# Performance work log

Hardware: AMD Instinct MI355X
Metric: run time of the kernel (lower is better)

Reference implementation:

```python
import jax, jax.numpy as jnp
import numpy as np

B, L, DIM = 4, 2048, 512
H, D = 8, 64
SCALE = D ** -0.5
NEG = -10000.0


def setup_inputs() -> dict:
    key = jax.random.key(0)
    ks = jax.random.split(key, 5)
    std = 1.0 / np.sqrt(DIM)
    return {
        "x": jax.random.normal(ks[0], (B, L, DIM), dtype=jnp.float32),
        "wq": jax.random.normal(ks[1], (H * D, DIM), dtype=jnp.float32) * std,
        "wk": jax.random.normal(ks[2], (H * D, DIM), dtype=jnp.float32) * std,
        "wv": jax.random.normal(ks[3], (H * D, DIM), dtype=jnp.float32) * std,
        "wo": jax.random.normal(ks[4], (DIM, H * D), dtype=jnp.float32) * std,
    }


def reference(x, wq, wk, wv, wo):
    b, l, _ = x.shape
    # projections (torch Linear: y = x @ W.T), split heads -> [b,h,l,d]
    q = (x @ wq.T).reshape(b, l, H, D).transpose(0, 2, 1, 3)
    k = (x @ wk.T).reshape(b, l, H, D).transpose(0, 2, 1, 3)
    v = (x @ wv.T).reshape(b, l, H, D).transpose(0, 2, 1, 3)
    scores = jnp.einsum("bhld,bhsd->bhls", q, k) * SCALE
    scores = jnp.nan_to_num(scores, nan=0.0, posinf=10000.0, neginf=NEG)
    diag = jnp.eye(l, dtype=bool)[None, None]  # [1,1,l,l]
    scores = jnp.where(diag, NEG, scores)
    attn = jax.nn.softmax(scores, axis=-1)
    attn = jnp.where(diag, 0.0, attn)
    attn = jnp.nan_to_num(attn, nan=0.0, posinf=0.0, neginf=0.0)
    out = jnp.einsum("bhls,bhsd->bhld", attn, v)
    out = out.transpose(0, 2, 1, 3).reshape(b, l, H * D)
    return out @ wo.T
```

## Files before the change

kernel.cpp:

```cpp
#include <hip/hip_runtime.h>
#include <hip/hip_bf16.h>


#define Bsz 4
#define Lsz 2048
#define DIMsz 512
#define Hsz 8
#define Dsz 64

typedef _Float16 f16;
typedef __attribute__((ext_vector_type(8))) _Float16 f16x8;
typedef __attribute__((ext_vector_type(4))) _Float16 f16x4;
typedef __attribute__((ext_vector_type(2))) __fp16 fp16x2;
typedef __attribute__((ext_vector_type(4))) float f32x4;
typedef __attribute__((ext_vector_type(16))) float f32x16;
typedef unsigned int u32;
typedef __attribute__((ext_vector_type(2))) unsigned int u32x2;

#if __has_builtin(__builtin_amdgcn_exp2f)
#define EXP2(x) __builtin_amdgcn_exp2f(x)
#else
#define EXP2(x) __expf(0.6931471805599453f * (x))
#endif

__device__ __forceinline__ u32 pack2(float a, float b) {
#if __has_builtin(__builtin_amdgcn_cvt_pkrtz)
    fp16x2 h = __builtin_amdgcn_cvt_pkrtz(a, b);
    return __builtin_bit_cast(u32, h);
#else
    fp16x2 h; h.x = (__fp16)a; h.y = (__fp16)b;
    return __builtin_bit_cast(u32, h);
#endif
}

#if __has_builtin(__builtin_amdgcn_permlane32_swap)
__device__ __forceinline__ void plswap(u32& a, u32& b) {
    u32x2 r = __builtin_amdgcn_permlane32_swap(a, b, false, false);
    a = r.x; b = r.y;
}
#else
__device__ __forceinline__ void plswap(u32& a, u32& b) {
    u32 sa = (u32)__shfl_xor((int)a, 32);
    u32 sb = (u32)__shfl_xor((int)b, 32);
    bool hi = (threadIdx.x & 32) != 0;
    u32 na = hi ? sb : a;
    u32 nb = hi ? b : sa;
    a = na; b = nb;
}
#endif

__device__ __forceinline__ void gl2lds16(const void* g, void* l) {
    __builtin_amdgcn_global_load_lds(
        (const __attribute__((address_space(1))) u32*)g,
        (__attribute__((address_space(3))) u32*)l, 16, 0, 0);
}

__global__ __launch_bounds__(256) void pack_f16(
    const float* __restrict__ x, const float* __restrict__ wq,
    const float* __restrict__ wk, const float* __restrict__ wv,
    const float* __restrict__ wo,
    f16* __restrict__ xh, f16* __restrict__ w3h, f16* __restrict__ woh)
{
    int bx = blockIdx.x, seg, blk;
    if (bx < 4096) { seg = 0; blk = bx; }
    else { seg = 1 + ((bx - 4096) >> 8); blk = (bx - 4096) & 255; }
    const float* s; f16* d; float sc = 1.0f;
    switch (seg) {
        case 0: s = x;  d = xh;            break;
        case 1: s = wq; d = w3h;           sc = 0.18033688011112042f; break;
        case 2: s = wk; d = w3h + 262144;  break;
        case 3: s = wv; d = w3h + 524288;  break;
        default: s = wo; d = woh;          break;
    }
    int i = (blk * 256 + threadIdx.x) * 4;
    float4 v = *(const float4*)(s + i);
    f16x4 o;
    o.x = (f16)(v.x * sc); o.y = (f16)(v.y * sc);
    o.z = (f16)(v.z * sc); o.w = (f16)(v.w * sc);
    *(f16x4*)(d + i) = o;
}

__global__ __launch_bounds__(256) void gemm_qkv_f16(
    const f16* __restrict__ A, const f16* __restrict__ B,
    f16* __restrict__ qh, f16* __restrict__ kh, f16* __restrict__ vth)
{
    __shared__ __align__(16) char smem[32768];
    f16* Ash = (f16*)smem;
    f16* Bsh = (f16*)(smem + 16384);

    const int tid = threadIdx.x;
    const int w = tid >> 6, lane = tid & 63;
    const int quad = lane >> 4, low = lane & 15;
    const int wm = w >> 1, wn = w & 1;
    const int m0 = blockIdx.y * 128, n0 = blockIdx.x * 128;

    f32x4 acc[4][4];
    #pragma unroll
    for (int i = 0; i < 4; i++)
        #pragma unroll
        for (int j = 0; j < 4; j++) acc[i][j] = (f32x4){0.f, 0.f, 0.f, 0.f};

    #pragma unroll 1
    for (int k0 = 0; k0 < DIMsz; k0 += 64) {
        __syncthreads();
        #pragma unroll
        for (int j = 0; j < 4; j++) {
            int t = j * 256 + tid;
            int r = t >> 3, g = t & 7;
            int gc = (g ^ (r & 7)) * 8;
            char* lb = (char*)Ash + (j * 256 + w * 64) * 16;
            gl2lds16(A + (size_t)(m0 + r) * DIMsz + k0 + gc, lb);
            char* lb2 = (char*)Bsh + (j * 256 + w * 64) * 16;
            gl2lds16(B + (size_t)(n0 + r) * DIMsz + k0 + gc, lb2);
        }
        __syncthreads();

        #pragma unroll
        for (int ks2 = 0; ks2 < 2; ks2++) {
            f16x8 af[4], bf[4];
            #pragma unroll
            for (int mt = 0; mt < 4; mt++) {
                int ar = wm * 64 + mt * 16 + low;
                int c = ks2 * 4 + quad;
                af[mt] = *(const f16x8*)&Ash[ar * 64 + ((c ^ (ar & 7)) << 3)];
            }
            #pragma unroll
            for (int nt = 0; nt < 4; nt++) {
                int br = wn * 64 + nt * 16 + low;
                int c = ks2 * 4 + quad;
                bf[nt] = *(const f16x8*)&Bsh[br * 64 + ((c ^ (br & 7)) << 3)];
            }
            #pragma unroll
            for (int mt = 0; mt < 4; mt++)
                #pragma unroll
                for (int nt = 0; nt < 4; nt++)
                    acc[mt][nt] = __builtin_amdgcn_mfma_f32_16x16x32_f16(
                        af[mt], bf[nt], acc[mt][nt], 0, 0, 0);
        }
    }

    const int proj = n0 >> 9;
    if (proj < 2) {
        f16* dst = (proj == 0) ? qh : kh;
        #pragma unroll
        for (int nt = 0; nt < 4; nt++) {
            int n = n0 + wn * 64 + nt * 16 + low;
            int c = n & 511, h = c >> 6, d = c & 63;
            #pragma unroll
            for (int mt = 0; mt < 4; mt++)
                #pragma unroll
                for (int r = 0; r < 4; r++) {
                    int m = m0 + wm * 64 + mt * 16 + quad * 4 + r;
                    int b_ = m >> 11, l = m & (Lsz - 1);
                    size_t bh = (size_t)(b_ * Hsz + h);
                    dst[(bh * Lsz + l) * Dsz + d] = (f16)acc[mt][nt][r];
                }
        }
    } else {
        const int hb = (n0 & 511) >> 6;
        f16* Tv = (f16*)smem;
        const int b_ = m0 >> 11, l0 = m0 & (Lsz - 1);
        #pragma unroll 1
        for (int hs = 0; hs < 2; hs++) {
            __syncthreads();
            if (wn == hs) {
                #pragma unroll
                for (int nt = 0; nt < 4; nt++) {
                    int d = nt * 16 + low;
                    #pragma unroll
                    for (int mt = 0; mt < 4; mt++)
                        #pragma unroll
                        for (int r = 0; r < 4; r++) {
                            int l = wm * 64 + mt * 16 + quad * 4 + r;
                            Tv[d * 136 + l] = (f16)acc[mt][nt][r];
                        }
                }
            }
            __syncthreads();
            int d = tid >> 2, seg = tid & 3;
            size_t bh = (size_t)(b_ * Hsz + hb + hs);
            f16* dstp = vth + (bh * 64 + d) * (size_t)Lsz + l0 + seg * 32;
            const f16* srcp = Tv + d * 136 + seg * 32;
            #pragma unroll
            for (int j = 0; j < 4; j++)
                *(f16x8*)(dstp + j * 8) = *(const f16x8*)(srcp + j * 8);
        }
    }
}

__global__ __launch_bounds__(256, 3) void attn_mfma(
    const f16* __restrict__ q, const f16* __restrict__ k,
    const f16* __restrict__ vt, f16* __restrict__ ctx)
{
    __shared__ __align__(16) char smem[32768];
    __shared__ float Ls[4][2][32];

    f16* Ks = (f16*)smem;
    f16* Vs = (f16*)(smem + 16384);

    const int tid = threadIdx.x;
    const int w = tid >> 6, lane = tid & 63;
    const int col = lane & 31;
    const int h = lane >> 5;
    const int bh = blockIdx.x;
    const int qb = blockIdx.y;
    const int q0 = qb * 64;
    const size_t kvb = (size_t)bh * Lsz;

    f16x8 qf[2][4];
    #pragma unroll
    for (int qt = 0; qt < 2; qt++)
        #pragma unroll
        for (int s = 0; s < 4; s++)
            qf[qt][s] = *(const f16x8*)(q + (kvb + q0 + qt * 32 + col) * Dsz
                                          + s * 16 + h * 8);

    const f16* kp; const f16* vp;
    {
        int rk = tid >> 3, gk = tid & 7;
        kp = k + (kvb + rk) * Dsz + ((gk ^ (rk & 7)) << 3);
        int rv = tid >> 4, gv = tid & 15;
        vp = vt + ((size_t)bh * Dsz + rv) * Lsz + ((gv ^ (rv & 15)) << 3);
    }
    char* kl = (char*)Ks + (w * 64) * 16;
    char* vl = (char*)Vs + (w * 64) * 16;

    const int rk = w * 32 + col;
    const f16* kfp[4];
    #pragma unroll
    for (int s = 0; s < 4; s++)
        kfp[s] = Ks + rk * 64 + (((s * 2 + h) ^ (rk & 7)) << 3);
    const f16* vfp[2][2];
    #pragma unroll
    for (int dt = 0; dt < 2; dt++)
        #pragma unroll
        for (int ks = 0; ks < 2; ks++) {
            int rv = dt * 32 + col, cv = w * 4 + ks * 2 + h;
            vfp[dt][ks] = Vs + rv * 128 + ((cv ^ (rv & 15)) << 3);
        }

    f32x16 acc[2][2];
    #pragma unroll
    for (int qt = 0; qt < 2; qt++)
        #pragma unroll
        for (int dt = 0; dt < 2; dt++)
            #pragma unroll
            for (int i = 0; i < 16; i++) acc[qt][dt][i] = 0.f;
    float lsum[2] = {0.f, 0.f};

    const int drd_s0 = (qb >> 1) * 128;
    const int dqt = w - (qb & 1) * 2;

    #pragma unroll 1
    for (int s0 = 0; s0 < Lsz; s0 += 128) {
        __syncthreads();
        gl2lds16(kp,        kl);
        gl2lds16(kp + 2048, kl + 4096);
        gl2lds16(kp + 4096, kl + 8192);
        gl2lds16(kp + 6144, kl + 12288);
        gl2lds16(vp,            vl);
        gl2lds16(vp + 16 * Lsz, vl + 4096);
        gl2lds16(vp + 32 * Lsz, vl + 8192);
        gl2lds16(vp + 48 * Lsz, vl + 12288);
        kp += 128 * Dsz;
        vp += 128;
        __syncthreads();

        f32x16 st[2];
        #pragma unroll
        for (int i = 0; i < 16; i++) { st[0][i] = 0.f; st[1][i] = 0.f; }
        #pragma unroll
        for (int s = 0; s < 4; s++) {
            f16x8 kf = *(const f16x8*)kfp[s];
            st[0] = __builtin_amdgcn_mfma_f32_32x32x16_f16(kf, qf[0][s], st[0], 0, 0, 0);
            st[1] = __builtin_amdgcn_mfma_f32_32x32x16_f16(kf, qf[1][s], st[1], 0, 0, 0);
        }

        union { u32 u[4]; f16x8 v; } pf[2][2];
        const bool drnd = (s0 == drd_s0);
        #pragma unroll
        for (int qt = 0; qt < 2; qt++) {
            float pv[16];
            #pragma unroll
            for (int i = 0; i < 16; i++) pv[i] = EXP2(st[qt][i]);
            if (drnd && qt == dqt) {
                #pragma unroll
                for (int i = 0; i < 16; i++) {
                    int row = (i & 3) + 8 * (i >> 2) + 4 * h;
                    pv[i] = (row == col) ? 0.f : pv[i];
                }
            }
            #pragma unroll
            for (int i = 0; i < 16; i++) lsum[qt] += pv[i];
            u32 P2[8];
            #pragma unroll
            for (int j = 0; j < 8; j++)
                P2[j] = pack2(pv[2 * j], pv[2 * j + 1]);
            plswap(P2[0], P2[2]); plswap(P2[1], P2[3]);
            plswap(P2[4], P2[6]); plswap(P2[5], P2[7]);
            #pragma unroll
            for (int jj = 0; jj < 4; jj++) {
                pf[qt][0].u[jj] = P2[jj];
                pf[qt][1].u[jj] = P2[4 + jj];
            }
        }

        #pragma unroll
        for (int dt = 0; dt < 2; dt++)
            #pragma unroll
            for (int ks = 0; ks < 2; ks++) {
                f16x8 vf = *(const f16x8*)vfp[dt][ks];
                acc[0][dt] = __builtin_amdgcn_mfma_f32_32x32x16_f16(
                    vf, pf[0][ks].v, acc[0][dt], 0, 0, 0);
                acc[1][dt] = __builtin_amdgcn_mfma_f32_32x32x16_f16(
                    vf, pf[1][ks].v, acc[1][dt], 0, 0, 0);
            }
    }

    #pragma unroll
    for (int qt = 0; qt < 2; qt++) {
        lsum[qt] += __shfl_xor(lsum[qt], 32);
        if (h == 0) Ls[w][qt][col] = lsum[qt];
    }

    float* Om = (float*)smem;
    __syncthreads();
    if (w == 1 || w == 3) {
        float* og = Om + (w >> 1) * 4096;
        #pragma unroll
        for (int qt = 0; qt < 2; qt++)
            #pragma unroll
            for (int dt = 0; dt < 2; dt++)
                #pragma unroll
                for (int i = 0; i < 16; i++) {
                    int row = (i & 3) + 8 * (i >> 2) + 4 * h;
                    og[(dt * 32 + row) * 64 + qt * 32 + col] = acc[qt][dt][i];
                }
    }
    __syncthreads();
    if (w == 0 || w == 2) {
        const float* og = Om + (w >> 1) * 4096;
        #pragma unroll
        for (int qt = 0; qt < 2; qt++)
            #pragma unroll
            for (int dt = 0; dt < 2; dt++)
                #pragma unroll
                for (int i = 0; i < 16; i++) {
                    int row = (i & 3) + 8 * (i >> 2) + 4 * h;
                    acc[qt][dt][i] += og[(dt * 32 + row) * 64 + qt * 32 + col];
                }
    }
    __syncthreads();
    if (w == 2) {
        #pragma unroll
        for (int qt = 0; qt < 2; qt++)
            #pragma unroll
            for (int dt = 0; dt < 2; dt++)
                #pragma unroll
                for (int i = 0; i < 16; i++) {
                    int row = (i & 3) + 8 * (i >> 2) + 4 * h;
                    Om[(dt * 32 + row) * 64 + qt * 32 + col] = acc[qt][dt][i];
                }
    }
    __syncthreads();
    if (w == 0) {
        #pragma unroll
        for (int qt = 0; qt < 2; qt++)
            #pragma unroll
            for (int dt = 0; dt < 2; dt++)
                #pragma unroll
                for (int i = 0; i < 16; i++) {
                    int row = (i & 3) + 8 * (i >> 2) + 4 * h;
                    acc[qt][dt][i] += Om[(dt * 32 + row) * 64 + qt * 32 + col];
                }
        const int b = bh >> 3, hh = bh & 7;
        #pragma unroll
        for (int qt = 0; qt < 2; qt++) {
            float ls = Ls[0][qt][col] + Ls[1][qt][col]
                     + Ls[2][qt][col] + Ls[3][qt][col];
            const float inv = 1.0f / ls;
            f16* op = ctx + ((size_t)(b * Lsz + q0 + qt * 32 + col)) * DIMsz
                          + hh * 64;
            #pragma unroll
            for (int dt = 0; dt < 2; dt++)
                #pragma unroll
                for (int r4 = 0; r4 < 4; r4++) {
                    f16x4 o;
                    o.x = (f16)(acc[qt][dt][4 * r4 + 0] * inv);
                    o.y = (f16)(acc[qt][dt][4 * r4 + 1] * inv);
                    o.z = (f16)(acc[qt][dt][4 * r4 + 2] * inv);
                    o.w = (f16)(acc[qt][dt][4 * r4 + 3] * inv);
                    *(f16x4*)(op + dt * 32 + 8 * r4 + 4 * h) = o;
                }
        }
    }
}

__global__ __launch_bounds__(256) void gemm_out_f16(
    const f16* __restrict__ A, const f16* __restrict__ B,
    float* __restrict__ C)
{
    __shared__ f16 Ash[64 * 64];
    __shared__ f16 Bsh[64 * 64];
    const int tid = threadIdx.x;
    const int w = tid >> 6, lane = tid & 63;
    const int quad = lane >> 4, low = lane & 15;
    const int wm = w >> 1, wn = w & 1;
    const int m0 = blockIdx.y * 64, n0 = blockIdx.x * 64;

    f32x4 acc[2][2];
    #pragma unroll
    for (int i = 0; i < 2; i++)
        #pragma unroll
        for (int j = 0; j < 2; j++) acc[i][j] = (f32x4){0.f, 0.f, 0.f, 0.f};

    #pragma unroll 1
    for (int k0 = 0; k0 < DIMsz; k0 += 64) {
        __syncthreads();
        #pragma unroll
        for (int j = 0; j < 2; j++) {
            int t = j * 256 + tid;
            int r = t >> 3, g = t & 7;
            int gc = (g ^ (r & 7)) * 8;
            char* lb = (char*)Ash + (j * 256 + w * 64) * 16;
            gl2lds16(A + (size_t)(m0 + r) * DIMsz + k0 + gc, lb);
            char* lb2 = (char*)Bsh + (j * 256 + w * 64) * 16;
            gl2lds16(B + (size_t)(n0 + r) * DIMsz + k0 + gc, lb2);
        }
        __syncthreads();

        #pragma unroll
        for (int ks2 = 0; ks2 < 2; ks2++) {
            f16x8 af[2], bf[2];
            #pragma unroll
            for (int mt = 0; mt < 2; mt++) {
                int ar = wm * 32 + mt * 16 + low;
                int c = ks2 * 4 + quad;
                af[mt] = *(const f16x8*)&Ash[ar * 64 + ((c ^ (ar & 7)) << 3)];
            }
            #pragma unroll
            for (int nt = 0; nt < 2; nt++) {
                int br = wn * 32 + nt * 16 + low;
                int c = ks2 * 4 + quad;
                bf[nt] = *(const f16x8*)&Bsh[br * 64 + ((c ^ (br & 7)) << 3)];
            }
            #pragma unroll
            for (int mt = 0; mt < 2; mt++)
                #pragma unroll
                for (int nt = 0; nt < 2; nt++)
                    acc[mt][nt] = __builtin_amdgcn_mfma_f32_16x16x32_f16(
                        af[mt], bf[nt], acc[mt][nt], 0, 0, 0);
        }
    }

    #pragma unroll
    for (int mt = 0; mt < 2; mt++)
        #pragma unroll
        for (int r = 0; r < 4; r++) {
            int m = m0 + wm * 32 + mt * 16 + quad * 4 + r;
            #pragma unroll
            for (int nt = 0; nt < 2; nt++) {
                int n = n0 + wn * 32 + nt * 16 + low;
                C[(size_t)m * DIMsz + n] = acc[mt][nt][r];
            }
        }
}

extern "C" void kernel_launch(void* const* d_in, const int* in_sizes, int n_in,
                              void* d_out, int out_size, void* d_ws, size_t ws_size,
                              hipStream_t stream) {
    const float* x  = (const float*)d_in[0];
    const float* wq = (const float*)d_in[1];
    const float* wk = (const float*)d_in[2];
    const float* wv = (const float*)d_in[3];
    const float* wo = (const float*)d_in[4];
    float* out = (float*)d_out;

    const size_t NTOK = (size_t)Bsz * Lsz;
    const size_t XSZ  = NTOK * DIMsz;

    f16* xh   = (f16*)d_ws;
    f16* w3h  = xh + XSZ;
    f16* woh  = w3h + 3 * 262144;
    f16* qh   = woh + 262144;
    f16* kh   = qh + XSZ;
    f16* vth  = kh + XSZ;
    f16* ctxh = vth + XSZ;

    pack_f16<<<5120, 256, 0, stream>>>(x, wq, wk, wv, wo, xh, w3h, woh);

    dim3 g1(1536 / 128, NTOK / 128);
    gemm_qkv_f16<<<g1, 256, 0, stream>>>(xh, w3h, qh, kh, vth);

    dim3 g2(Bsz * Hsz, Lsz / 64);
    attn_mfma<<<g2, 256, 0, stream>>>(qh, kh, vth, ctxh);

    dim3 g3(DIMsz / 64, NTOK / 64);
    gemm_out_f16<<<g3, 256, 0, stream>>>(ctxh, woh, out);
}
```

Baseline: 166.6 us.

## Double-buffer K/V LDS tiles in attention and sum probabilities via fdot2

```diff
diff --git a/kernel.cpp b/kernel.cpp
--- a/kernel.cpp
+++ b/kernel.cpp
@@ -30,6 +30,16 @@
 #else
     fp16x2 h; h.x = (__fp16)a; h.y = (__fp16)b;
     return __builtin_bit_cast(u32, h);
+#endif
+}
+
+__device__ __forceinline__ float addpair(u32 p, float c) {
+#if __has_builtin(__builtin_amdgcn_fdot2)
+    fp16x2 ones; ones.x = (__fp16)1.0f; ones.y = (__fp16)1.0f;
+    return __builtin_amdgcn_fdot2(__builtin_bit_cast(fp16x2, p), ones, c, false);
+#else
+    fp16x2 h = __builtin_bit_cast(fp16x2, p);
+    return c + (float)h.x + (float)h.y;
 #endif
 }
 
@@ -188,15 +198,12 @@
     }
 }
 
-__global__ __launch_bounds__(256, 3) void attn_mfma(
+__global__ __launch_bounds__(256, 2) void attn_mfma(
     const f16* __restrict__ q, const f16* __restrict__ k,
     const f16* __restrict__ vt, f16* __restrict__ ctx)
 {
-    __shared__ __align__(16) char smem[32768];
+    __shared__ __align__(16) char smem[65536];
     __shared__ float Ls[4][2][32];
-
-    f16* Ks = (f16*)smem;
-    f16* Vs = (f16*)(smem + 16384);
 
     const int tid = threadIdx.x;
     const int w = tid >> 6, lane = tid & 63;
@@ -222,22 +229,28 @@
         int rv = tid >> 4, gv = tid & 15;
         vp = vt + ((size_t)bh * Dsz + rv) * Lsz + ((gv ^ (rv & 15)) << 3);
     }
-    char* kl = (char*)Ks + (w * 64) * 16;
-    char* vl = (char*)Vs + (w * 64) * 16;
-
+
+    char* kl[2]; char* vl[2];
+    const f16* kfp[2][4];
+    const f16* vfp[2][2][2];
     const int rk = w * 32 + col;
-    const f16* kfp[4];
-    #pragma unroll
-    for (int s = 0; s < 4; s++)
-        kfp[s] = Ks + rk * 64 + (((s * 2 + h) ^ (rk & 7)) << 3);
-    const f16* vfp[2][2];
-    #pragma unroll
-    for (int dt = 0; dt < 2; dt++)
-        #pragma unroll
-        for (int ks = 0; ks < 2; ks++) {
-            int rv = dt * 32 + col, cv = w * 4 + ks * 2 + h;
-            vfp[dt][ks] = Vs + rv * 128 + ((cv ^ (rv & 15)) << 3);
-        }
+    #pragma unroll
+    for (int b = 0; b < 2; b++) {
+        f16* Ks = (f16*)(smem + b * 32768);
+        f16* Vs = (f16*)(smem + b * 32768 + 16384);
+        kl[b] = (char*)Ks + (w * 64) * 16;
+        vl[b] = (char*)Vs + (w * 64) * 16;
+        #pragma unroll
+        for (int s = 0; s < 4; s++)
+            kfp[b][s] = Ks + rk * 64 + (((s * 2 + h) ^ (rk & 7)) << 3);
+        #pragma unroll
+        for (int dt = 0; dt < 2; dt++)
+            #pragma unroll
+            for (int ks = 0; ks < 2; ks++) {
+                int rv = dt * 32 + col, cv = w * 4 + ks * 2 + h;
+                vfp[b][dt][ks] = Vs + rv * 128 + ((cv ^ (rv & 15)) << 3);
+            }
+    }
 
     f32x16 acc[2][2];
     #pragma unroll
@@ -248,36 +261,48 @@
             for (int i = 0; i < 16; i++) acc[qt][dt][i] = 0.f;
     float lsum[2] = {0.f, 0.f};
 
-    const int drd_s0 = (qb >> 1) * 128;
+    const int drnd_i = qb >> 1;
     const int dqt = w - (qb & 1) * 2;
 
+    gl2lds16(kp,        kl[0]);
+    gl2lds16(kp + 2048, kl[0] + 4096);
+    gl2lds16(kp + 4096, kl[0] + 8192);
+    gl2lds16(kp + 6144, kl[0] + 12288);
+    gl2lds16(vp,            vl[0]);
+    gl2lds16(vp + 16 * Lsz, vl[0] + 4096);
+    gl2lds16(vp + 32 * Lsz, vl[0] + 8192);
+    gl2lds16(vp + 48 * Lsz, vl[0] + 12288);
+    kp += 128 * Dsz; vp += 128;
+    __syncthreads();
+
+    int b = 0;
     #pragma unroll 1
-    for (int s0 = 0; s0 < Lsz; s0 += 128) {
-        __syncthreads();
-        gl2lds16(kp,        kl);
-        gl2lds16(kp + 2048, kl + 4096);
-        gl2lds16(kp + 4096, kl + 8192);
-        gl2lds16(kp + 6144, kl + 12288);
-        gl2lds16(vp,            vl);
-        gl2lds16(vp + 16 * Lsz, vl + 4096);
-        gl2lds16(vp + 32 * Lsz, vl + 8192);
-        gl2lds16(vp + 48 * Lsz, vl + 12288);
-        kp += 128 * Dsz;
-        vp += 128;
-        __syncthreads();
+    for (int r = 0; r < 16; r++) {
+        if (r < 15) {
+            char* knl = kl[b ^ 1]; char* vnl = vl[b ^ 1];
+            gl2lds16(kp,        knl);
+            gl2lds16(kp + 2048, knl + 4096);
+            gl2lds16(kp + 4096, knl + 8192);
+            gl2lds16(kp + 6144, knl + 12288);
+            gl2lds16(vp,            vnl);
+            gl2lds16(vp + 16 * Lsz, vnl + 4096);
+            gl2lds16(vp + 32 * Lsz, vnl + 8192);
+            gl2lds16(vp + 48 * Lsz, vnl + 12288);
+            kp += 128 * Dsz; vp += 128;
+        }
 
         f32x16 st[2];
         #pragma unroll
         for (int i = 0; i < 16; i++) { st[0][i] = 0.f; st[1][i] = 0.f; }
         #pragma unroll
         for (int s = 0; s < 4; s++) {
-            f16x8 kf = *(const f16x8*)kfp[s];
+            f16x8 kf = *(const f16x8*)kfp[b][s];
             st[0] = __builtin_amdgcn_mfma_f32_32x32x16_f16(kf, qf[0][s], st[0], 0, 0, 0);
             st[1] = __builtin_amdgcn_mfma_f32_32x32x16_f16(kf, qf[1][s], st[1], 0, 0, 0);
         }
 
         union { u32 u[4]; f16x8 v; } pf[2][2];
-        const bool drnd = (s0 == drd_s0);
+        const bool drnd = (r == drnd_i);
         #pragma unroll
         for (int qt = 0; qt < 2; qt++) {
             float pv[16];
@@ -290,12 +315,12 @@
                     pv[i] = (row == col) ? 0.f : pv[i];
                 }
             }
-            #pragma unroll
-            for (int i = 0; i < 16; i++) lsum[qt] += pv[i];
             u32 P2[8];
             #pragma unroll
-            for (int j = 0; j < 8; j++)
+            for (int j = 0; j < 8; j++) {
                 P2[j] = pack2(pv[2 * j], pv[2 * j + 1]);
+                lsum[qt] = addpair(P2[j], lsum[qt]);
+            }
             plswap(P2[0], P2[2]); plswap(P2[1], P2[3]);
             plswap(P2[4], P2[6]); plswap(P2[5], P2[7]);
             #pragma unroll
@@ -309,12 +334,15 @@
         for (int dt = 0; dt < 2; dt++)
             #pragma unroll
             for (int ks = 0; ks < 2; ks++) {
-                f16x8 vf = *(const f16x8*)vfp[dt][ks];
+                f16x8 vf = *(const f16x8*)vfp[b][dt][ks];
                 acc[0][dt] = __builtin_amdgcn_mfma_f32_32x32x16_f16(
                     vf, pf[0][ks].v, acc[0][dt], 0, 0, 0);
                 acc[1][dt] = __builtin_amdgcn_mfma_f32_32x32x16_f16(
                     vf, pf[1][ks].v, acc[1][dt], 0, 0, 0);
             }
+
+        __syncthreads();
+        b ^= 1;
     }
 
     #pragma unroll
@@ -373,13 +401,13 @@
                     int row = (i & 3) + 8 * (i >> 2) + 4 * h;
                     acc[qt][dt][i] += Om[(dt * 32 + row) * 64 + qt * 32 + col];
                 }
-        const int b = bh >> 3, hh = bh & 7;
+        const int bb = bh >> 3, hh = bh & 7;
         #pragma unroll
         for (int qt = 0; qt < 2; qt++) {
             float ls = Ls[0][qt][col] + Ls[1][qt][col]
                      + Ls[2][qt][col] + Ls[3][qt][col];
             const float inv = 1.0f / ls;
-            f16* op = ctx + ((size_t)(b * Lsz + q0 + qt * 32 + col)) * DIMsz
+            f16* op = ctx + ((size_t)(bb * Lsz + q0 + qt * 32 + col)) * DIMsz
                           + hh * 64;
             #pragma unroll
             for (int dt = 0; dt < 2; dt++)
```

After: 172.3 us. 3.4% more time.
